# Optimization experiments

Hardware: AMD Instinct MI355X
Metric: run time of the kernel (lower is better)

## Reference

```python
import jax, jax.numpy as jnp
import numpy as np
from jax import lax

STRIDE = 1
PADDING = 1


def setup_inputs() -> dict:
    key = jax.random.key(0)
    kx, kw = jax.random.split(key)
    x = jax.random.normal(kx, (32, 64, 64, 64), dtype=jnp.float32)
    # weights are angles uniform on (-pi, pi)
    weight = jax.random.uniform(kw, (128, 64, 3, 3), dtype=jnp.float32,
                                minval=-jnp.pi, maxval=jnp.pi)
    return {"x": x, "weight": weight}


def _ring_conv2d(x, weight, stride, padding):
    # out[b,o,i,j] = sum_{c,kh,kw} cos(x_pad[b,c,i*s+kh,j*s+kw] - w[o,c,kh,kw])
    # cos(a-b) = cos a cos b + sin a sin b  ->  two standard convolutions.
    # Pad the raw angles with zeros first (a padded zero contributes cos(-w)).
    p = padding
    xp = jnp.pad(x, ((0, 0), (0, 0), (p, p), (p, p)))
    dn = ('NCHW', 'OIHW', 'NCHW')
    out = lax.conv_general_dilated(jnp.cos(xp), jnp.cos(weight),
                                   window_strides=(stride, stride),
                                   padding='VALID', dimension_numbers=dn)
    out = out + lax.conv_general_dilated(jnp.sin(xp), jnp.sin(weight),
                                         window_strides=(stride, stride),
                                         padding='VALID', dimension_numbers=dn)
    return out


def reference(x, weight):
    return _ring_conv2d(x, weight, STRIDE, PADDING)
```

## Files before the change

### kernel.cpp

```cpp
#include <hip/hip_runtime.h>
#include <hip/hip_bf16.h>


typedef _Float16 half8 __attribute__((ext_vector_type(8)));
typedef float f32x16 __attribute__((ext_vector_type(16)));

#define NB 32
#define NC 64
#define NH 64
#define NW 64
#define NO 128
#define PW 66
#define PSTRIDE 72
#define TPX 204

union U16 { unsigned short u; _Float16 h; };
union HB { uint4 u4; unsigned long long q[2]; half8 h; };

__device__ inline unsigned pack_cs(float ang) {
    float s, c;
    sincosf(ang, &s, &c);
    U16 uc, us; uc.h = (_Float16)c; us.h = (_Float16)s;
    return (unsigned)uc.u | ((unsigned)us.u << 16);
}

__device__ inline unsigned pack_cs_fast(float ang) {
    float s, c;
    __sincosf(ang, &s, &c);
    U16 uc, us; uc.h = (_Float16)c; us.h = (_Float16)s;
    return (unsigned)uc.u | ((unsigned)us.u << 16);
}

__global__ __launch_bounds__(256) void prep_x(const float* __restrict__ x,
                                              uint4* __restrict__ xp) {
    __shared__ unsigned ls[64 * 65];
    const int b = blockIdx.x >> 6, row = blockIdx.x & 63;
    const int t = threadIdx.x;
#pragma unroll
    for (int pass = 0; pass < 16; ++pass) {
        int c = pass * 4 + (t >> 6);
        int col = t & 63;
        float v = x[((size_t)(b * NC + c) * NH + row) * NW + col];
        ls[c * 65 + col] = pack_cs_fast(v);
    }
    __syncthreads();
    const int q = t & 3, col = t >> 2;
#pragma unroll
    for (int cg = 0; cg < 4; ++cg) {
        uint4 vv;
        vv.x = ls[(cg * 16 + 4 * q + 0) * 65 + col];
        vv.y = ls[(cg * 16 + 4 * q + 1) * 65 + col];
        vv.z = ls[(cg * 16 + 4 * q + 2) * 65 + col];
        vv.w = ls[(cg * 16 + 4 * q + 3) * 65 + col];
        xp[(size_t)(((b * 4 + cg) * PW + row + 1) * PW + col + 1) * 4 + q] = vv;
    }
}

__global__ __launch_bounds__(256) void prep_border(uint4* __restrict__ xp) {
    const int bc = blockIdx.x;
    uint4* base = xp + (size_t)bc * PW * PW * 4;
    const uint4 v = make_uint4(0x3C00u, 0x3C00u, 0x3C00u, 0x3C00u);
    for (int idx = threadIdx.x; idx < 260 * 4; idx += 256) {
        int p = idx >> 2, q = idx & 3;
        int r, c;
        if (p < 66)       { r = 0;       c = p; }
        else if (p < 132) { r = 65;      c = p - 66; }
        else if (p < 196) { r = p - 131; c = 0; }
        else              { r = p - 195; c = 65; }
        base[(size_t)(r * PW + c) * 4 + q] = v;
    }
}

__global__ __launch_bounds__(256) void prep_w(const float* __restrict__ w,
                                              uint4* __restrict__ wqa) {
    int t = blockIdx.x * 256 + threadIdx.x;
    if (t >= 36 * 2 * 128 * 2) return;
    int g2 = t & 1, o = (t >> 1) & 127, kk = (t >> 8) & 1, chunk = t >> 9;
    int cg = chunk / 9, kpos = chunk % 9, kh = kpos / 3, kw = kpos % 3;
    unsigned r[4];
#pragma unroll
    for (int m = 0; m < 4; ++m) {
        int c = cg * 16 + kk * 8 + g2 * 4 + m;
        float ang = w[((o * NC + c) * 3 + kh) * 3 + kw];
        r[m] = pack_cs(ang);
    }
    wqa[t] = make_uint4(r[0], r[1], r[2], r[3]);
}

__global__ __launch_bounds__(256, 3) void ring_conv(const uint4* __restrict__ xp,
                                                    const uint4* __restrict__ wqa,
                                                    float* __restrict__ out) {
    __shared__ __align__(16) char xs[TPX * PSTRIDE];

    const int d = blockIdx.x;
    const int blk = (d & 7) * 128 + (d >> 3);

    const int ch = blk & 1, rq = (blk >> 1) & 15, b = blk >> 5;
    const int row0 = rq * 4, col0 = ch * 32;

    const int t = threadIdx.x, lane = t & 63, wid = t >> 6;
    const int l31 = lane & 31, g2 = lane >> 5;

    f32x16 acc[4] = {};

    int goff[4], loff[4];
#pragma unroll
    for (int k = 0; k < 4; ++k) {
        int e = k * 256 + t;
        if (e > 815) e = 815;
        int p = e >> 2, q = e & 3;
        int rr = p / 34, cc = p - rr * 34;
        goff[k] = ((row0 + rr) * PW + (col0 + cc)) * 4 + q;
        loff[k] = p * PSTRIDE + q * 16;
    }
    const size_t img_stride = (size_t)PW * PW * 4;
    const uint4* img0 = xp + (size_t)(b * 4) * img_stride;

    const int xlane = l31 * PSTRIDE + g2 * 16;
    const int aoff = (wid * 32 + l31) * 2 + g2;

    {
        uint4 S[4];
#pragma unroll
        for (int k = 0; k < 4; ++k) S[k] = img0[goff[k]];
#pragma unroll
        for (int k = 0; k < 4; ++k) {
            char* dst = xs + loff[k];
            *(unsigned long long*)dst = (unsigned long long)S[k].x | ((unsigned long long)S[k].y << 32);
            *(unsigned long long*)(dst + 8) = (unsigned long long)S[k].z | ((unsigned long long)S[k].w << 32);
        }
    }
    __syncthreads();

    for (int cg = 0; cg < 4; ++cg) {
        uint4 S[4];
        if (cg < 3) {
            const uint4* img = img0 + (size_t)(cg + 1) * img_stride;
#pragma unroll
            for (int k = 0; k < 4; ++k) S[k] = img[goff[k]];
        }

        const uint4* wa = wqa + (size_t)(cg * 9 * 2) * 256 + aoff;

        HB Aop[2], Bop[2][4];
        Aop[0].u4 = wa[0];
        Aop[1].u4 = wa[256];
#pragma unroll
        for (int r = 0; r < 4; ++r) {
            const char* sp = xs + r * 34 * PSTRIDE + xlane;
            Bop[0][r].q[0] = *(const unsigned long long*)sp;
            Bop[0][r].q[1] = *(const unsigned long long*)(sp + 8);
        }

#pragma unroll
        for (int s = 0; s < 18; ++s) {
            const int cp = s & 1, np = cp ^ 1;
            if (s < 17) {
                const int s1 = s + 1, kp1 = s1 >> 1, kk1 = s1 & 1;
                const int kh1 = kp1 / 3, kw1 = kp1 % 3;
#pragma unroll
                for (int r = 0; r < 4; ++r) {
                    const char* sp = xs + (((r + kh1) * 34 + kw1) * PSTRIDE + kk1 * 32) + xlane;
                    Bop[np][r].q[0] = *(const unsigned long long*)sp;
                    Bop[np][r].q[1] = *(const unsigned long long*)(sp + 8);
                }
            }
            __builtin_amdgcn_s_setprio(1);
#pragma unroll
            for (int r = 0; r < 4; ++r)
                acc[r] = __builtin_amdgcn_mfma_f32_32x32x16_f16(Aop[cp].h, Bop[cp][r].h,
                                                                acc[r], 0, 0, 0);
            __builtin_amdgcn_s_setprio(0);
            if (s < 16) Aop[cp].u4 = wa[(s + 2) * 256];
        }

        __syncthreads();
        if (cg < 3) {
#pragma unroll
            for (int k = 0; k < 4; ++k) {
                char* dst = xs + loff[k];
                *(unsigned long long*)dst = (unsigned long long)S[k].x | ((unsigned long long)S[k].y << 32);
                *(unsigned long long*)(dst + 8) = (unsigned long long)S[k].z | ((unsigned long long)S[k].w << 32);
            }
        }
        __syncthreads();
    }

#pragma unroll
    for (int r = 0; r < 4; ++r) {
        const int orow = row0 + r;
#pragma unroll
        for (int reg = 0; reg < 16; ++reg) {
            int o = wid * 32 + (reg & 3) + 8 * (reg >> 2) + 4 * g2;
            out[(((size_t)b * NO + o) * NH + orow) * NW + col0 + l31] = acc[r][reg];
        }
    }
}

extern "C" void kernel_launch(void* const* d_in, const int* in_sizes, int n_in,
                              void* d_out, int out_size, void* d_ws, size_t ws_size,
                              hipStream_t stream) {
    const float* x = (const float*)d_in[0];
    const float* w = (const float*)d_in[1];

    uint4* xpnt = (uint4*)d_ws;
    uint4* wqp = (uint4*)((char*)d_ws + (size_t)36 * 1024 * 1024);

    prep_border<<<NB * 4, 256, 0, stream>>>(xpnt);
    prep_x<<<NB * NH, 256, 0, stream>>>(x, xpnt);
    prep_w<<<72, 256, 0, stream>>>(w, wqp);
    ring_conv<<<1024, 256, 0, stream>>>(xpnt, wqp, (float*)d_out);
}
```

Measured before the change: 68.07 us.

## Fuse prep kernels and enlarge conv tile to 8 rows with 2x64 outputs per wave

```diff
diff --git a/kernel.cpp b/kernel.cpp
--- a/kernel.cpp
+++ b/kernel.cpp
@@ -12,7 +12,9 @@
 #define NO 128
 #define PW 66
 #define PSTRIDE 72
-#define TPX 204
+#define TROWS 10
+#define TCOLS 34
+#define TPX (TROWS * TCOLS)
 
 union U16 { unsigned short u; _Float16 h; };
 union HB { uint4 u4; unsigned long long q[2]; half8 h; };
@@ -31,85 +33,89 @@
     return (unsigned)uc.u | ((unsigned)us.u << 16);
 }
 
-__global__ __launch_bounds__(256) void prep_x(const float* __restrict__ x,
-                                              uint4* __restrict__ xp) {
+__global__ __launch_bounds__(256) void prep_all(const float* __restrict__ x,
+                                                const float* __restrict__ w,
+                                                uint4* __restrict__ xp,
+                                                uint4* __restrict__ wqa) {
     __shared__ unsigned ls[64 * 65];
-    const int b = blockIdx.x >> 6, row = blockIdx.x & 63;
+    const int blk = blockIdx.x;
     const int t = threadIdx.x;
-#pragma unroll
-    for (int pass = 0; pass < 16; ++pass) {
-        int c = pass * 4 + (t >> 6);
-        int col = t & 63;
-        float v = x[((size_t)(b * NC + c) * NH + row) * NW + col];
-        ls[c * 65 + col] = pack_cs_fast(v);
-    }
-    __syncthreads();
-    const int q = t & 3, col = t >> 2;
-#pragma unroll
-    for (int cg = 0; cg < 4; ++cg) {
-        uint4 vv;
-        vv.x = ls[(cg * 16 + 4 * q + 0) * 65 + col];
-        vv.y = ls[(cg * 16 + 4 * q + 1) * 65 + col];
-        vv.z = ls[(cg * 16 + 4 * q + 2) * 65 + col];
-        vv.w = ls[(cg * 16 + 4 * q + 3) * 65 + col];
-        xp[(size_t)(((b * 4 + cg) * PW + row + 1) * PW + col + 1) * 4 + q] = vv;
-    }
-}
-
-__global__ __launch_bounds__(256) void prep_border(uint4* __restrict__ xp) {
-    const int bc = blockIdx.x;
-    uint4* base = xp + (size_t)bc * PW * PW * 4;
-    const uint4 v = make_uint4(0x3C00u, 0x3C00u, 0x3C00u, 0x3C00u);
-    for (int idx = threadIdx.x; idx < 260 * 4; idx += 256) {
-        int p = idx >> 2, q = idx & 3;
-        int r, c;
-        if (p < 66)       { r = 0;       c = p; }
-        else if (p < 132) { r = 65;      c = p - 66; }
-        else if (p < 196) { r = p - 131; c = 0; }
-        else              { r = p - 195; c = 65; }
-        base[(size_t)(r * PW + c) * 4 + q] = v;
-    }
-}
-
-__global__ __launch_bounds__(256) void prep_w(const float* __restrict__ w,
-                                              uint4* __restrict__ wqa) {
-    int t = blockIdx.x * 256 + threadIdx.x;
-    if (t >= 36 * 2 * 128 * 2) return;
-    int g2 = t & 1, o = (t >> 1) & 127, kk = (t >> 8) & 1, chunk = t >> 9;
-    int cg = chunk / 9, kpos = chunk % 9, kh = kpos / 3, kw = kpos % 3;
-    unsigned r[4];
-#pragma unroll
-    for (int m = 0; m < 4; ++m) {
-        int c = cg * 16 + kk * 8 + g2 * 4 + m;
-        float ang = w[((o * NC + c) * 3 + kh) * 3 + kw];
-        r[m] = pack_cs(ang);
-    }
-    wqa[t] = make_uint4(r[0], r[1], r[2], r[3]);
-}
-
-__global__ __launch_bounds__(256, 3) void ring_conv(const uint4* __restrict__ xp,
+
+    if (blk < NB * NH) {
+        const int b = blk >> 6, row = blk & 63;
+#pragma unroll
+        for (int pass = 0; pass < 16; ++pass) {
+            int c = pass * 4 + (t >> 6);
+            int col = t & 63;
+            float v = x[((size_t)(b * NC + c) * NH + row) * NW + col];
+            ls[c * 65 + col] = pack_cs_fast(v);
+        }
+        __syncthreads();
+        const int q = t & 3, col = t >> 2;
+#pragma unroll
+        for (int cg = 0; cg < 4; ++cg) {
+            uint4 vv;
+            vv.x = ls[(cg * 16 + 4 * q + 0) * 65 + col];
+            vv.y = ls[(cg * 16 + 4 * q + 1) * 65 + col];
+            vv.z = ls[(cg * 16 + 4 * q + 2) * 65 + col];
+            vv.w = ls[(cg * 16 + 4 * q + 3) * 65 + col];
+            xp[(size_t)(((b * 4 + cg) * PW + row + 1) * PW + col + 1) * 4 + q] = vv;
+        }
+    } else if (blk < NB * NH + 72) {
+        int tt = (blk - NB * NH) * 256 + t;
+        if (tt < 36 * 2 * 128 * 2) {
+            int g2 = tt & 1, o = (tt >> 1) & 127, kk = (tt >> 8) & 1, chunk = tt >> 9;
+            int cg = chunk / 9, kpos = chunk % 9, kh = kpos / 3, kw = kpos % 3;
+            unsigned r[4];
+#pragma unroll
+            for (int m = 0; m < 4; ++m) {
+                int c = cg * 16 + kk * 8 + g2 * 4 + m;
+                float ang = w[((o * NC + c) * 3 + kh) * 3 + kw];
+                r[m] = pack_cs(ang);
+            }
+            wqa[tt] = make_uint4(r[0], r[1], r[2], r[3]);
+        }
+    } else {
+        const int bc = blk - NB * NH - 72;
+        uint4* base = xp + (size_t)bc * PW * PW * 4;
+        const uint4 v = make_uint4(0x3C00u, 0x3C00u, 0x3C00u, 0x3C00u);
+        for (int idx = t; idx < 260 * 4; idx += 256) {
+            int p = idx >> 2, q = idx & 3;
+            int r, c;
+            if (p < 66)       { r = 0;       c = p; }
+            else if (p < 132) { r = 65;      c = p - 66; }
+            else if (p < 196) { r = p - 131; c = 0; }
+            else              { r = p - 195; c = 65; }
+            base[(size_t)(r * PW + c) * 4 + q] = v;
+        }
+    }
+}
+
+__global__ __launch_bounds__(256, 2) void ring_conv(const uint4* __restrict__ xp,
                                                     const uint4* __restrict__ wqa,
                                                     float* __restrict__ out) {
     __shared__ __align__(16) char xs[TPX * PSTRIDE];
 
     const int d = blockIdx.x;
-    const int blk = (d & 7) * 128 + (d >> 3);
-
-    const int ch = blk & 1, rq = (blk >> 1) & 15, b = blk >> 5;
-    const int row0 = rq * 4, col0 = ch * 32;
+    const int blk = (d & 7) * 64 + (d >> 3);
+
+    const int ch = blk & 1, rq = (blk >> 1) & 7, b = blk >> 4;
+    const int row0 = rq * 8, col0 = ch * 32;
 
     const int t = threadIdx.x, lane = t & 63, wid = t >> 6;
     const int l31 = lane & 31, g2 = lane >> 5;
-
-    f32x16 acc[4] = {};
-
-    int goff[4], loff[4];
-#pragma unroll
-    for (int k = 0; k < 4; ++k) {
+    const int op = wid & 1, rg = wid >> 1;
+    const int rowbase = rg * 4;
+
+    f32x16 acc[2][4] = {};
+
+    int goff[6], loff[6];
+#pragma unroll
+    for (int k = 0; k < 6; ++k) {
         int e = k * 256 + t;
-        if (e > 815) e = 815;
+        if (e > TPX * 4 - 1) e = TPX * 4 - 1;
         int p = e >> 2, q = e & 3;
-        int rr = p / 34, cc = p - rr * 34;
+        int rr = p / TCOLS, cc = p - rr * TCOLS;
         goff[k] = ((row0 + rr) * PW + (col0 + cc)) * 4 + q;
         loff[k] = p * PSTRIDE + q * 16;
     }
@@ -117,14 +123,14 @@
     const uint4* img0 = xp + (size_t)(b * 4) * img_stride;
 
     const int xlane = l31 * PSTRIDE + g2 * 16;
-    const int aoff = (wid * 32 + l31) * 2 + g2;
+    const uint4* wbase = wqa + (op * 64 + l31) * 2 + g2;
 
     {
-        uint4 S[4];
-#pragma unroll
-        for (int k = 0; k < 4; ++k) S[k] = img0[goff[k]];
-#pragma unroll
-        for (int k = 0; k < 4; ++k) {
+        uint4 S[6];
+#pragma unroll
+        for (int k = 0; k < 6; ++k) S[k] = img0[goff[k]];
+#pragma unroll
+        for (int k = 0; k < 6; ++k) {
             char* dst = xs + loff[k];
             *(unsigned long long*)dst = (unsigned long long)S[k].x | ((unsigned long long)S[k].y << 32);
             *(unsigned long long*)(dst + 8) = (unsigned long long)S[k].z | ((unsigned long long)S[k].w << 32);
@@ -133,23 +139,27 @@
     __syncthreads();
 
     for (int cg = 0; cg < 4; ++cg) {
-        uint4 S[4];
+        const uint4* wa = wbase + (size_t)(cg * 18) * 256;
+
+        HB Ar[4][2];
+#pragma unroll
+        for (int i = 0; i < 4; ++i) {
+            Ar[i][0].u4 = wa[i * 256];
+            Ar[i][1].u4 = wa[i * 256 + 64];
+        }
+        HB Bop[2][4];
+#pragma unroll
+        for (int r = 0; r < 4; ++r) {
+            const char* sp = xs + (rowbase + r) * TCOLS * PSTRIDE + xlane;
+            Bop[0][r].q[0] = *(const unsigned long long*)sp;
+            Bop[0][r].q[1] = *(const unsigned long long*)(sp + 8);
+        }
+
+        uint4 S[6];
         if (cg < 3) {
             const uint4* img = img0 + (size_t)(cg + 1) * img_stride;
 #pragma unroll
-            for (int k = 0; k < 4; ++k) S[k] = img[goff[k]];
-        }
-
-        const uint4* wa = wqa + (size_t)(cg * 9 * 2) * 256 + aoff;
-
-        HB Aop[2], Bop[2][4];
-        Aop[0].u4 = wa[0];
-        Aop[1].u4 = wa[256];
-#pragma unroll
-        for (int r = 0; r < 4; ++r) {
-            const char* sp = xs + r * 34 * PSTRIDE + xlane;
-            Bop[0][r].q[0] = *(const unsigned long long*)sp;
-            Bop[0][r].q[1] = *(const unsigned long long*)(sp + 8);
+            for (int k = 0; k < 6; ++k) S[k] = img[goff[k]];
         }
 
 #pragma unroll
@@ -160,7 +170,8 @@
                 const int kh1 = kp1 / 3, kw1 = kp1 % 3;
 #pragma unroll
                 for (int r = 0; r < 4; ++r) {
-                    const char* sp = xs + (((r + kh1) * 34 + kw1) * PSTRIDE + kk1 * 32) + xlane;
+                    const char* sp = xs
+                        + (((rowbase + r + kh1) * TCOLS + kw1) * PSTRIDE + kk1 * 32) + xlane;
                     Bop[np][r].q[0] = *(const unsigned long long*)sp;
                     Bop[np][r].q[1] = *(const unsigned long long*)(sp + 8);
                 }
@@ -168,33 +179,40 @@
             __builtin_amdgcn_s_setprio(1);
 #pragma unroll
             for (int r = 0; r < 4; ++r)
-                acc[r] = __builtin_amdgcn_mfma_f32_32x32x16_f16(Aop[cp].h, Bop[cp][r].h,
-                                                                acc[r], 0, 0, 0);
+#pragma unroll
+                for (int f = 0; f < 2; ++f)
+                    acc[f][r] = __builtin_amdgcn_mfma_f32_32x32x16_f16(
+                        Ar[s & 3][f].h, Bop[cp][r].h, acc[f][r], 0, 0, 0);
             __builtin_amdgcn_s_setprio(0);
-            if (s < 16) Aop[cp].u4 = wa[(s + 2) * 256];
+            if (s < 14) {
+                Ar[s & 3][0].u4 = wa[(s + 4) * 256];
+                Ar[s & 3][1].u4 = wa[(s + 4) * 256 + 64];
+            }
         }
 
         __syncthreads();
         if (cg < 3) {
 #pragma unroll
-            for (int k = 0; k < 4; ++k) {
+            for (int k = 0; k < 6; ++k) {
                 char* dst = xs + loff[k];
                 *(unsigned long long*)dst = (unsigned long long)S[k].x | ((unsigned long long)S[k].y << 32);
                 *(unsigned long long*)(dst + 8) = (unsigned long long)S[k].z | ((unsigned long long)S[k].w << 32);
             }
-        }
-        __syncthreads();
-    }
-
-#pragma unroll
-    for (int r = 0; r < 4; ++r) {
-        const int orow = row0 + r;
-#pragma unroll
-        for (int reg = 0; reg < 16; ++reg) {
-            int o = wid * 32 + (reg & 3) + 8 * (reg >> 2) + 4 * g2;
-            out[(((size_t)b * NO + o) * NH + orow) * NW + col0 + l31] = acc[r][reg];
-        }
-    }
+            __syncthreads();
+        }
+    }
+
+#pragma unroll
+    for (int f = 0; f < 2; ++f)
+#pragma unroll
+        for (int r = 0; r < 4; ++r) {
+            const int orow = row0 + rowbase + r;
+#pragma unroll
+            for (int reg = 0; reg < 16; ++reg) {
+                int o = op * 64 + f * 32 + (reg & 3) + 8 * (reg >> 2) + 4 * g2;
+                out[(((size_t)b * NO + o) * NH + orow) * NW + col0 + l31] = acc[f][r][reg];
+            }
+        }
 }
 
 extern "C" void kernel_launch(void* const* d_in, const int* in_sizes, int n_in,
@@ -206,8 +224,6 @@
     uint4* xpnt = (uint4*)d_ws;
     uint4* wqp = (uint4*)((char*)d_ws + (size_t)36 * 1024 * 1024);
 
-    prep_border<<<NB * 4, 256, 0, stream>>>(xpnt);
-    prep_x<<<NB * NH, 256, 0, stream>>>(x, xpnt);
-    prep_w<<<72, 256, 0, stream>>>(w, wqp);
-    ring_conv<<<1024, 256, 0, stream>>>(xpnt, wqp, (float*)d_out);
-}
+    prep_all<<<NB * NH + 72 + 128, 256, 0, stream>>>(x, w, xpnt, wqp);
+    ring_conv<<<512, 256, 0, stream>>>(xpnt, wqp, (float*)d_out);
+}
```

New measurement: 57.26 us, median of 3. 1.19x faster.
